# Optimization experiments

Measured on AMD Instinct MI355X. Metric: run time of the kernel, lower is better.

Reference implementation:

```python
import jax, jax.numpy as jnp
import numpy as np

B, R, D, H, L, E, NREL = 8, 1024, 256, 8, 2, 32768, 32
FF = 4 * D
HD = D // H
NEG = -1e9  # finite 'masked' value (stands in for -inf in the sparse attention mask)


def setup_inputs() -> dict:
    key = jax.random.key(0)
    ks = jax.random.split(key, 18)
    s = 0.02
    inp = {
        'node_embeddings': jax.random.normal(ks[0], (B, R, D), jnp.float32),
        'edge_index': jax.random.randint(ks[1], (B, 2, E), 0, R, jnp.int32),
        'relation_id': jax.random.randint(ks[2], (B, E), 0, NREL, jnp.int32),
        'keep_mask': jax.random.randint(ks[3], (B, E), 0, 2, jnp.int32).astype(bool),
        # learned params
        'rel_bias': jax.random.normal(ks[4], (max(NREL, 32), 1), jnp.float32) * s,
        'Wqkv': jax.random.normal(ks[5], (L, 3 * D, D), jnp.float32) * s,
        'bqkv': jnp.zeros((L, 3 * D), jnp.float32),
        'Wo': jax.random.normal(ks[6], (L, D, D), jnp.float32) * s,
        'bo': jnp.zeros((L, D), jnp.float32),
        'ln1_g': jnp.ones((L, D), jnp.float32),
        'ln1_b': jnp.zeros((L, D), jnp.float32),
        'W1': jax.random.normal(ks[7], (L, FF, D), jnp.float32) * s,
        'b1': jnp.zeros((L, FF), jnp.float32),
        'W2': jax.random.normal(ks[8], (L, D, FF), jnp.float32) * s,
        'b2': jnp.zeros((L, D), jnp.float32),
        'ln2_g': jnp.ones((L, D), jnp.float32),
        'ln2_b': jnp.zeros((L, D), jnp.float32),
    }
    return inp


def _layer_norm(x, g, b, eps=1e-5):
    mu = jnp.mean(x, axis=-1, keepdims=True)
    var = jnp.mean(jnp.square(x - mu), axis=-1, keepdims=True)
    return (x - mu) * jax.lax.rsqrt(var + eps) * g + b


def _build_mask(edge_index, relation_id, keep_mask, rel_bias):
    # Vectorized equivalent of the per-batch / per-edge Python loops:
    # base mask: NEG everywhere, 0 at kept edges (and diagonal), then scatter-ADD
    # the per-edge relation bias (duplicate edges accumulate, as in the loop).
    src = edge_index[:, 0, :]  # [B,E]
    dst = edge_index[:, 1, :]  # [B,E]
    bidx = jnp.broadcast_to(jnp.arange(B)[:, None], (B, E))
    mask = jnp.full((B, R, R), NEG, jnp.float32)
    base_vals = jnp.where(keep_mask, 0.0, NEG)
    mask = mask.at[bidx, src, dst].max(base_vals)  # dropped edges leave NEG
    di = jnp.arange(R)
    mask = mask.at[:, di, di].set(0.0)  # self-attention always allowed
    bias = rel_bias[relation_id, 0]  # [B,E]
    mask = mask.at[bidx, src, dst].add(jnp.where(keep_mask, bias, 0.0))
    return mask


def reference(node_embeddings, edge_index, relation_id, keep_mask, rel_bias,
              Wqkv, bqkv, Wo, bo, ln1_g, ln1_b, W1, b1, W2, b2, ln2_g, ln2_b):
    mask = _build_mask(edge_index, relation_id, keep_mask, rel_bias)  # [B,R,R]
    x = node_embeddings
    scale = 1.0 / np.sqrt(HD).astype(np.float32)
    for l in range(L):
        qkv = jnp.einsum('brd,ed->bre', x, Wqkv[l]) + bqkv[l]
        q, k, v = jnp.split(qkv, 3, axis=-1)
        q = q.reshape(B, R, H, HD)
        k = k.reshape(B, R, H, HD)
        v = v.reshape(B, R, H, HD)
        scores = jnp.einsum('bqhd,bkhd->bhqk', q, k) * scale + mask[:, None]
        attn = jax.nn.softmax(scores, axis=-1)
        out = jnp.einsum('bhqk,bkhd->bqhd', attn, v).reshape(B, R, D)
        out = jnp.einsum('brd,ed->bre', out, Wo[l]) + bo[l]
        x = _layer_norm(x + out, ln1_g[l], ln1_b[l])
        h = jax.nn.gelu(jnp.einsum('brd,fd->brf', x, W1[l]) + b1[l], approximate=False)
        h = jnp.einsum('brf,df->brd', h, W2[l]) + b2[l]
        x = _layer_norm(x + h, ln2_g[l], ln2_b[l])
    return x
```

## Files before the change

### kernel.cpp

```cpp
#include <hip/hip_runtime.h>
#include <hip/hip_bf16.h>
#include <math.h>

#define B_ 8
#define R_ 1024
#define D_ 256
#define H_ 8
#define L_ 2
#define E_ 32768
#define FF_ 1024
#define NEGV (-1000000000.0f)

typedef short bf16x8 __attribute__((ext_vector_type(8)));
typedef float f32x4 __attribute__((ext_vector_type(4)));

__device__ __forceinline__ unsigned short f2b(float f){
  unsigned int u = __float_as_uint(f);
  u += 0x7fffu + ((u >> 16) & 1u);
  return (unsigned short)(u >> 16);
}

__device__ __forceinline__ unsigned int pk_bf16(float lo, float hi){
  unsigned int r;
  asm volatile("v_cvt_pk_bf16_f32 %0, %1, %2" : "=v"(r) : "v"(lo), "v"(hi));
  return r;
}

#define ASYNC_COPY16(gp, lp) \
  __builtin_amdgcn_global_load_lds((const __attribute__((address_space(1))) void*)(gp), \
                                   (__attribute__((address_space(3))) void*)(lp), 16, 0, 0)


__global__ void detect_bool(const unsigned char* __restrict__ km, int* __restrict__ flag){
  int i = blockIdx.x*256 + threadIdx.x;
  int hit = ((i & 3) != 0) && (km[i] != 0);
  if (__ballot(hit) != 0ull && (threadIdx.x & 63) == 0) atomicOr(flag, 1);
}

__global__ void mask_fill(float* __restrict__ mask){
  size_t i = ((size_t)blockIdx.x*256 + threadIdx.x)*4;
  int row = (int)((i >> 10) & 1023);
  int col = (int)(i & 1023);
  float4 v;
  v.x = (row == col+0) ? 0.0f : NEGV;
  v.y = (row == col+1) ? 0.0f : NEGV;
  v.z = (row == col+2) ? 0.0f : NEGV;
  v.w = (row == col+3) ? 0.0f : NEGV;
  *(float4*)&mask[i] = v;
}

__device__ __forceinline__ int keep_of(const unsigned char* km, const int* flag, int tid){
  return flag[0] ? (int)km[tid] : (int)km[(size_t)tid*4];
}

__global__ void edge_base(const int* __restrict__ ei, const unsigned char* __restrict__ km,
                          const int* __restrict__ flag, float* __restrict__ mask){
  int tid = blockIdx.x*256 + threadIdx.x;
  int b = tid >> 15, e = tid & (E_-1);
  if (keep_of(km, flag, tid)){
    int src = ei[(size_t)b*2*E_ + e];
    int dst = ei[(size_t)b*2*E_ + E_ + e];
    mask[((size_t)b*R_ + src)*R_ + dst] = 0.0f;
  }
}

__global__ void edge_bias(const int* __restrict__ ei, const int* __restrict__ rid,
                          const unsigned char* __restrict__ km, const int* __restrict__ flag,
                          const float* __restrict__ rb, float* __restrict__ mask){
  int tid = blockIdx.x*256 + threadIdx.x;
  int b = tid >> 15, e = tid & (E_-1);
  if (keep_of(km, flag, tid)){
    int src = ei[(size_t)b*2*E_ + e];
    int dst = ei[(size_t)b*2*E_ + E_ + e];
    atomicAdd(&mask[((size_t)b*R_ + src)*R_ + dst], rb[rid[tid]]);
  }
}


__global__ void cvt_bf16(const float* __restrict__ src, unsigned short* __restrict__ dst, int n){
  int i = (blockIdx.x*256 + threadIdx.x)*4;
  if (i >= n) return;
  float4 v = *(const float4*)&src[i];
  ushort4 o;
  o.x = f2b(v.x); o.y = f2b(v.y); o.z = f2b(v.z); o.w = f2b(v.w);
  *(ushort4*)&dst[i] = o;
}

template<int MODE, int BN>
__global__ __launch_bounds__(256) void gemm_bt(const unsigned short* __restrict__ A,
    const unsigned short* __restrict__ Bw, const float* __restrict__ bias,
    void* __restrict__ Cout, int M, int N, int K)
{
  constexpr int NI = BN/32;
  constexpr int NCH = 8 + BN/16;
  constexpr int CPW = NCH/4;
  __shared__ unsigned short As[128*32];
  __shared__ unsigned short Bs[BN*32];
  const int nb = N / BN;
  const int bm = blockIdx.x / nb, bn = blockIdx.x % nb;
  const int m0 = bm << 7, n0 = bn * BN;
  const int t = threadIdx.x, lane = t & 63, wid = t >> 6;
  const int wr = wid >> 1, wc = wid & 1;
  const int c = lane & 15, g = lane >> 4;

  f32x4 zz = {0.f,0.f,0.f,0.f};
  f32x4 acc[4][NI];
  #pragma unroll
  for (int mi=0; mi<4; mi++)
    #pragma unroll
    for (int ni=0; ni<NI; ni++) acc[mi][ni] = zz;

  for (int k0 = 0; k0 < K; k0 += 32){
    __syncthreads();
    #pragma unroll
    for (int it=0; it<CPW; ++it){
      int chunk = wid*CPW + it;
      int row16 = lane >> 2, seg = lane & 3;
      if (chunk < 8){
        int row = chunk*16 + row16;
        ASYNC_COPY16(A + (size_t)(m0+row)*K + k0 + seg*8, &As[chunk*512]);
      } else {
        int bch = chunk - 8;
        int row = bch*16 + row16;
        ASYNC_COPY16(Bw + (size_t)(n0+row)*K + k0 + seg*8, &Bs[bch*512]);
      }
    }
    __syncthreads();
    bf16x8 af[4], bfr[NI];
    #pragma unroll
    for (int mi=0; mi<4; mi++) af[mi]  = *(const bf16x8*)&As[(wr*64 + mi*16 + c)*32 + g*8];
    #pragma unroll
    for (int ni=0; ni<NI; ni++) bfr[ni] = *(const bf16x8*)&Bs[(wc*(BN/2) + ni*16 + c)*32 + g*8];
    #pragma unroll
    for (int mi=0; mi<4; mi++)
      #pragma unroll
      for (int ni=0; ni<NI; ni++)
        acc[mi][ni] = __builtin_amdgcn_mfma_f32_16x16x32_bf16(af[mi], bfr[ni], acc[mi][ni], 0,0,0);
  }

  #pragma unroll
  for (int mi=0; mi<4; mi++){
    #pragma unroll
    for (int ni=0; ni<NI; ni++){
      int col = n0 + wc*(BN/2) + ni*16 + c;
      float bv = bias[col];
      #pragma unroll
      for (int r=0; r<4; r++){
        int row = m0 + wr*64 + mi*16 + 4*g + r;
        float v = acc[mi][ni][r] + bv;
        if (MODE == 2) v = 0.5f*v*(1.0f + erff(v*0.70710678f));
        if (MODE == 1) ((float*)Cout)[(size_t)row*N + col] = v;
        else           ((unsigned short*)Cout)[(size_t)row*N + col] = f2b(v);
      }
    }
  }
}

__global__ __launch_bounds__(512, 4) void attn_kernel(const unsigned short* __restrict__ qkv,
    const float* __restrict__ mask, unsigned short* __restrict__ aout)
{
  __shared__ unsigned short Klds[128*40];
  __shared__ unsigned short VT[32*136];
  const int blk = blockIdx.x;
  const int qt = blk & 7, h = (blk >> 3) & 7, b = blk >> 6;
  const int t = threadIdx.x, lane = t & 63, w = t >> 6;
  const int c = lane & 15, g = lane >> 4;
  const int qrow = qt*128 + w*16 + c;
  const size_t qbase = (size_t)b*R_*768;
  const float scale = 0.17677669529663689f;

  bf16x8 qf = *(const bf16x8*)&qkv[qbase + (size_t)qrow*768 + h*32 + g*8];

  f32x4 z4 = {0.f,0.f,0.f,0.f};
  f32x4 oacc[2] = {z4, z4};
  float mrun = -1e30f, lrun = 0.f;

  const int srcA = c + ((lane & 16) << 1);
  const int srcB = srcA + 16;
  const bool hig = (lane >= 32);

  for (int kt=0; kt<8; ++kt){
    const int kv0 = kt*128;
    __syncthreads();
    {
      int row = t >> 2, seg = t & 3;
      uint4 kd = *(const uint4*)&qkv[qbase + (size_t)(kv0+row)*768 + 256 + h*32 + seg*8];
      *(uint4*)&Klds[row*40 + seg*8] = kd;
    }
    {
      int d = t & 31, grp = t >> 5;
      __align__(16) unsigned short tv[8];
      #pragma unroll
      for (int j=0; j<8; j++)
        tv[j] = qkv[qbase + (size_t)(kv0 + grp*8 + j)*768 + 512 + h*32 + d];
      *(uint4*)&VT[d*136 + grp*8] = *(const uint4*)&tv[0];
    }
    __syncthreads();

    f32x4 st[8];
    #pragma unroll
    for (int fc=0; fc<8; ++fc){
      bf16x8 kb = *(const bf16x8*)&Klds[(fc*16 + c)*40 + g*8];
      st[fc] = __builtin_amdgcn_mfma_f32_16x16x32_bf16(kb, qf, z4, 0,0,0);
    }
    const float* mrow = &mask[((size_t)b*R_ + qrow)*R_ + kv0];
    #pragma unroll
    for (int fc=0; fc<8; ++fc){
      float4 mv = *(const float4*)&mrow[fc*16 + 4*g];
      st[fc][0] = st[fc][0]*scale + mv.x;
      st[fc][1] = st[fc][1]*scale + mv.y;
      st[fc][2] = st[fc][2]*scale + mv.z;
      st[fc][3] = st[fc][3]*scale + mv.w;
    }
    float mx = st[0][0];
    #pragma unroll
    for (int fc=0; fc<8; ++fc)
      #pragma unroll
      for (int r=0; r<4; r++) mx = fmaxf(mx, st[fc][r]);
    mx = fmaxf(mx, __shfl_xor(mx, 16));
    mx = fmaxf(mx, __shfl_xor(mx, 32));
    float mnew  = fmaxf(mrun, mx);
    float alpha = __expf(mrun - mnew);
    float sum = 0.f;
    #pragma unroll
    for (int fc=0; fc<8; ++fc)
      #pragma unroll
      for (int r=0; r<4; r++){
        float pv = __expf(st[fc][r] - mnew);
        st[fc][r] = pv;
        sum += pv;
      }
    sum += __shfl_xor(sum, 16);
    sum += __shfl_xor(sum, 32);
    lrun = lrun*alpha + sum;
    mrun = mnew;
    oacc[0][0]*=alpha; oacc[0][1]*=alpha; oacc[0][2]*=alpha; oacc[0][3]*=alpha;
    oacc[1][0]*=alpha; oacc[1][1]*=alpha; oacc[1][2]*=alpha; oacc[1][3]*=alpha;

    unsigned int u0[8], u1[8];
    #pragma unroll
    for (int fc=0; fc<8; ++fc){
      u0[fc] = pk_bf16(st[fc][0], st[fc][1]);
      u1[fc] = pk_bf16(st[fc][2], st[fc][3]);
    }

    #pragma unroll
    for (int ks=0; ks<4; ++ks){
      unsigned int e0 = u0[2*ks],   e1 = u1[2*ks];
      unsigned int o0 = u0[2*ks+1], o1 = u1[2*ks+1];
      unsigned int w0e = __shfl((int)e0, srcA), w1e = __shfl((int)e1, srcA);
      unsigned int w2e = __shfl((int)e0, srcB), w3e = __shfl((int)e1, srcB);
      unsigned int w0o = __shfl((int)o0, srcA), w1o = __shfl((int)o1, srcA);
      unsigned int w2o = __shfl((int)o0, srcB), w3o = __shfl((int)o1, srcB);
      union { unsigned int u[4]; bf16x8 v; } pa;
      pa.u[0] = hig ? w0o : w0e;
      pa.u[1] = hig ? w1o : w1e;
      pa.u[2] = hig ? w2o : w2e;
      pa.u[3] = hig ? w3o : w3e;
      #pragma unroll
      for (int dg=0; dg<2; ++dg){
        bf16x8 vb = *(const bf16x8*)&VT[(dg*16 + c)*136 + ks*32 + g*8];
        oacc[dg] = __builtin_amdgcn_mfma_f32_16x16x32_bf16(vb, pa.v, oacc[dg], 0,0,0);
      }
    }
  }
  float rl = 1.0f / lrun;
  #pragma unroll
  for (int dg=0; dg<2; ++dg){
    unsigned int p0 = pk_bf16(oacc[dg][0]*rl, oacc[dg][1]*rl);
    unsigned int p1 = pk_bf16(oacc[dg][2]*rl, oacc[dg][3]*rl);
    size_t base = ((size_t)b*R_ + qrow)*D_ + h*32 + dg*16 + 4*g;
    uint2 pp; pp.x = p0; pp.y = p1;
    *(uint2*)&aout[base] = pp;
  }
}

__global__ __launch_bounds__(256) void resid_ln(const float* __restrict__ xin,
    const float* __restrict__ res, const float* __restrict__ gg, const float* __restrict__ bb,
    float* __restrict__ xout, unsigned short* __restrict__ xbf)
{
  int row = blockIdx.x*4 + (threadIdx.x >> 6);
  int lane = threadIdx.x & 63;
  size_t base = (size_t)row*D_ + lane*4;
  float4 a  = *(const float4*)&xin[base];
  float4 rr = *(const float4*)&res[base];
  float y0 = a.x+rr.x, y1 = a.y+rr.y, y2 = a.z+rr.z, y3 = a.w+rr.w;
  float s = y0+y1+y2+y3;
  #pragma unroll
  for (int off=32; off>=1; off>>=1) s += __shfl_xor(s, off);
  float mu = s * (1.0f/256.0f);
  float d0=y0-mu, d1=y1-mu, d2=y2-mu, d3=y3-mu;
  float q = d0*d0 + d1*d1 + d2*d2 + d3*d3;
  #pragma unroll
  for (int off=32; off>=1; off>>=1) q += __shfl_xor(q, off);
  float rstd = rsqrtf(q*(1.0f/256.0f) + 1e-5f);
  float4 gv = *(const float4*)&gg[lane*4];
  float4 bv = *(const float4*)&bb[lane*4];
  float o0 = d0*rstd*gv.x + bv.x;
  float o1 = d1*rstd*gv.y + bv.y;
  float o2 = d2*rstd*gv.z + bv.z;
  float o3 = d3*rstd*gv.w + bv.w;
  float4 o; o.x=o0; o.y=o1; o.z=o2; o.w=o3;
  *(float4*)&xout[base] = o;
  ushort4 ob; ob.x=f2b(o0); ob.y=f2b(o1); ob.z=f2b(o2); ob.w=f2b(o3);
  *(ushort4*)&xbf[base] = ob;
}

extern "C" void kernel_launch(void* const* d_in, const int* in_sizes, int n_in,
                              void* d_out, int out_size, void* d_ws, size_t ws_size,
                              hipStream_t stream)
{
  const float* node = (const float*)d_in[0];
  const int*   ei   = (const int*)d_in[1];
  const int*   rid  = (const int*)d_in[2];
  const unsigned char* km = (const unsigned char*)d_in[3];
  const float* rb   = (const float*)d_in[4];
  const float* Wqkv = (const float*)d_in[5];
  const float* bqkv = (const float*)d_in[6];
  const float* Wo   = (const float*)d_in[7];
  const float* bo   = (const float*)d_in[8];
  const float* ln1g = (const float*)d_in[9];
  const float* ln1b = (const float*)d_in[10];
  const float* W1   = (const float*)d_in[11];
  const float* b1   = (const float*)d_in[12];
  const float* W2   = (const float*)d_in[13];
  const float* b2   = (const float*)d_in[14];
  const float* ln2g = (const float*)d_in[15];
  const float* ln2b = (const float*)d_in[16];

  char* ws = (char*)d_ws;
  int*   flag = (int*)ws;
  float* mask = (float*)(ws + 256);
  unsigned short* wqkv_b = (unsigned short*)(ws + 33554688);
  unsigned short* wo_b   = (unsigned short*)(ws + 34341120);
  unsigned short* w1_b   = (unsigned short*)(ws + 34603264);
  unsigned short* w2_b   = (unsigned short*)(ws + 35651840);
  unsigned short* x_bf   = (unsigned short*)(ws + 36700416);
  unsigned short* qkvb   = (unsigned short*)(ws + 40894720);
  unsigned short* ao     = (unsigned short*)(ws + 53477632);
  float* xf   = (float*)(ws + 57671936);
  float* tmp  = (float*)(ws + 66060544);
  unsigned short* hbuf   = (unsigned short*)(ws + 74449152);

  hipMemsetAsync(flag, 0, 4, stream);
  detect_bool<<<1024, 256, 0, stream>>>(km, flag);
  mask_fill<<<8192, 256, 0, stream>>>(mask);
  edge_base<<<1024, 256, 0, stream>>>(ei, km, flag, mask);
  edge_bias<<<1024, 256, 0, stream>>>(ei, rid, km, flag, rb, mask);

  cvt_bf16<<<384, 256, 0, stream>>>(Wqkv, wqkv_b, L_*768*256);
  cvt_bf16<<<128, 256, 0, stream>>>(Wo,   wo_b,   L_*256*256);
  cvt_bf16<<<512, 256, 0, stream>>>(W1,   w1_b,   L_*1024*256);
  cvt_bf16<<<512, 256, 0, stream>>>(W2,   w2_b,   L_*256*1024);
  cvt_bf16<<<2048,256, 0, stream>>>(node, x_bf,   B_*R_*D_);

  for (int l = 0; l < L_; ++l){
    gemm_bt<0,128><<<384, 256, 0, stream>>>(x_bf, wqkv_b + l*196608, bqkv + l*768, qkvb, 8192, 768, 256);
    attn_kernel<<<512, 512, 0, stream>>>(qkvb, mask, ao);
    gemm_bt<1,64><<<256, 256, 0, stream>>>(ao, wo_b + l*65536, bo + l*256, tmp, 8192, 256, 256);
    resid_ln<<<2048, 256, 0, stream>>>(l==0 ? node : xf, tmp, ln1g + l*256, ln1b + l*256, xf, x_bf);
    gemm_bt<2,128><<<512, 256, 0, stream>>>(x_bf, w1_b + l*262144, b1 + l*1024, hbuf, 8192, 1024, 256);
    gemm_bt<1,64><<<256, 256, 0, stream>>>(hbuf, w2_b + l*262144, b2 + l*256, tmp, 8192, 256, 1024);
    float* outp = (l == L_-1) ? (float*)d_out : xf;
    resid_ln<<<2048, 256, 0, stream>>>(xf, tmp, ln2g + l*256, ln2b + l*256, outp, x_bf);
  }
}
```

Before: 341.7 us.

## Convert mask to bf16, split attention KV in halves, split-K output GEMMs

Converts the dense fp32 mask to bf16 once so attention reads half the mask bytes. Attention now splits the key range into two halves per block, which doubles the block count; a new merge kernel combines the partials using the saved running max and sum. The Wo and W2 GEMMs use split-K=2 with bf16 partial outputs, and a new residual+layernorm kernel sums the two partials and adds the bias. It also changes LDS padding and aliases workspace buffers. The extra passes and bf16 partials add memory traffic and rounding error in exchange for more parallelism and less mask bandwidth.

```diff
diff --git a/kernel.cpp b/kernel.cpp
--- a/kernel.cpp
+++ b/kernel.cpp
@@ -19,7 +19,9 @@
   u += 0x7fffu + ((u >> 16) & 1u);
   return (unsigned short)(u >> 16);
 }
-
+__device__ __forceinline__ float b2f(unsigned short u){
+  return __uint_as_float((unsigned int)u << 16);
+}
 __device__ __forceinline__ unsigned int pk_bf16(float lo, float hi){
   unsigned int r;
   asm volatile("v_cvt_pk_bf16_f32 %0, %1, %2" : "=v"(r) : "v"(lo), "v"(hi));
@@ -86,7 +88,7 @@
   *(ushort4*)&dst[i] = o;
 }
 
-template<int MODE, int BN>
+template<int MODE, int BN, int KS>
 __global__ __launch_bounds__(256) void gemm_bt(const unsigned short* __restrict__ A,
     const unsigned short* __restrict__ Bw, const float* __restrict__ bias,
     void* __restrict__ Cout, int M, int N, int K)
@@ -96,9 +98,12 @@
   constexpr int CPW = NCH/4;
   __shared__ unsigned short As[128*32];
   __shared__ unsigned short Bs[BN*32];
-  const int nb = N / BN;
-  const int bm = blockIdx.x / nb, bn = blockIdx.x % nb;
+  const int nb = N / BN, mb = M >> 7;
+  const int ks = blockIdx.x / (mb*nb);
+  const int rem = blockIdx.x % (mb*nb);
+  const int bm = rem / nb, bn = rem % nb;
   const int m0 = bm << 7, n0 = bn * BN;
+  const int kbeg = ks * (K/KS), kend = kbeg + K/KS;
   const int t = threadIdx.x, lane = t & 63, wid = t >> 6;
   const int wr = wid >> 1, wc = wid & 1;
   const int c = lane & 15, g = lane >> 4;
@@ -110,7 +115,7 @@
     #pragma unroll
     for (int ni=0; ni<NI; ni++) acc[mi][ni] = zz;
 
-  for (int k0 = 0; k0 < K; k0 += 32){
+  for (int k0 = kbeg; k0 < kend; k0 += 32){
     __syncthreads();
     #pragma unroll
     for (int it=0; it<CPW; ++it){
@@ -138,31 +143,32 @@
         acc[mi][ni] = __builtin_amdgcn_mfma_f32_16x16x32_bf16(af[mi], bfr[ni], acc[mi][ni], 0,0,0);
   }
 
+  unsigned short* outb = (unsigned short*)Cout + (size_t)ks*M*N;
   #pragma unroll
   for (int mi=0; mi<4; mi++){
     #pragma unroll
     for (int ni=0; ni<NI; ni++){
       int col = n0 + wc*(BN/2) + ni*16 + c;
-      float bv = bias[col];
+      float bv = (MODE == 1) ? 0.0f : bias[col];
       #pragma unroll
       for (int r=0; r<4; r++){
         int row = m0 + wr*64 + mi*16 + 4*g + r;
         float v = acc[mi][ni][r] + bv;
         if (MODE == 2) v = 0.5f*v*(1.0f + erff(v*0.70710678f));
-        if (MODE == 1) ((float*)Cout)[(size_t)row*N + col] = v;
-        else           ((unsigned short*)Cout)[(size_t)row*N + col] = f2b(v);
+        outb[(size_t)row*N + col] = f2b(v);
       }
     }
   }
 }
 
 __global__ __launch_bounds__(512, 4) void attn_kernel(const unsigned short* __restrict__ qkv,
-    const float* __restrict__ mask, unsigned short* __restrict__ aout)
+    const unsigned short* __restrict__ maskbf, unsigned short* __restrict__ po,
+    float* __restrict__ ml)
 {
-  __shared__ unsigned short Klds[128*40];
-  __shared__ unsigned short VT[32*136];
+  __shared__ unsigned short Klds[128*36];
+  __shared__ unsigned short VT[32*132];
   const int blk = blockIdx.x;
-  const int qt = blk & 7, h = (blk >> 3) & 7, b = blk >> 6;
+  const int half = blk & 1, qt = (blk >> 1) & 7, h = (blk >> 4) & 7, b = blk >> 7;
   const int t = threadIdx.x, lane = t & 63, w = t >> 6;
   const int c = lane & 15, g = lane >> 4;
   const int qrow = qt*128 + w*16 + c;
@@ -179,13 +185,13 @@
   const int srcB = srcA + 16;
   const bool hig = (lane >= 32);
 
-  for (int kt=0; kt<8; ++kt){
-    const int kv0 = kt*128;
+  for (int kt=0; kt<4; ++kt){
+    const int kv0 = half*512 + kt*128;
     __syncthreads();
     {
       int row = t >> 2, seg = t & 3;
       uint4 kd = *(const uint4*)&qkv[qbase + (size_t)(kv0+row)*768 + 256 + h*32 + seg*8];
-      *(uint4*)&Klds[row*40 + seg*8] = kd;
+      *(uint4*)&Klds[row*36 + seg*8] = kd;
     }
     {
       int d = t & 31, grp = t >> 5;
@@ -193,24 +199,24 @@
       #pragma unroll
       for (int j=0; j<8; j++)
         tv[j] = qkv[qbase + (size_t)(kv0 + grp*8 + j)*768 + 512 + h*32 + d];
-      *(uint4*)&VT[d*136 + grp*8] = *(const uint4*)&tv[0];
+      *(uint4*)&VT[d*132 + grp*8] = *(const uint4*)&tv[0];
     }
     __syncthreads();
 
     f32x4 st[8];
     #pragma unroll
     for (int fc=0; fc<8; ++fc){
-      bf16x8 kb = *(const bf16x8*)&Klds[(fc*16 + c)*40 + g*8];
+      bf16x8 kb = *(const bf16x8*)&Klds[(fc*16 + c)*36 + g*8];
       st[fc] = __builtin_amdgcn_mfma_f32_16x16x32_bf16(kb, qf, z4, 0,0,0);
     }
-    const float* mrow = &mask[((size_t)b*R_ + qrow)*R_ + kv0];
+    const unsigned short* mrow = &maskbf[((size_t)b*R_ + qrow)*R_ + kv0];
     #pragma unroll
     for (int fc=0; fc<8; ++fc){
-      float4 mv = *(const float4*)&mrow[fc*16 + 4*g];
-      st[fc][0] = st[fc][0]*scale + mv.x;
-      st[fc][1] = st[fc][1]*scale + mv.y;
-      st[fc][2] = st[fc][2]*scale + mv.z;
-      st[fc][3] = st[fc][3]*scale + mv.w;
+      ushort4 mu = *(const ushort4*)&mrow[fc*16 + 4*g];
+      st[fc][0] = st[fc][0]*scale + b2f(mu.x);
+      st[fc][1] = st[fc][1]*scale + b2f(mu.y);
+      st[fc][2] = st[fc][2]*scale + b2f(mu.z);
+      st[fc][3] = st[fc][3]*scale + b2f(mu.w);
     }
     float mx = st[0][0];
     #pragma unroll
@@ -243,7 +249,6 @@
       u0[fc] = pk_bf16(st[fc][0], st[fc][1]);
       u1[fc] = pk_bf16(st[fc][2], st[fc][3]);
     }
-
     #pragma unroll
     for (int ks=0; ks<4; ++ks){
       unsigned int e0 = u0[2*ks],   e1 = u1[2*ks];
@@ -259,32 +264,72 @@
       pa.u[3] = hig ? w3o : w3e;
       #pragma unroll
       for (int dg=0; dg<2; ++dg){
-        bf16x8 vb = *(const bf16x8*)&VT[(dg*16 + c)*136 + ks*32 + g*8];
+        bf16x8 vb = *(const bf16x8*)&VT[(dg*16 + c)*132 + ks*32 + g*8];
         oacc[dg] = __builtin_amdgcn_mfma_f32_16x16x32_bf16(vb, pa.v, oacc[dg], 0,0,0);
       }
     }
   }
-  float rl = 1.0f / lrun;
+  unsigned short* poh = po + (size_t)half*B_*R_*D_;
   #pragma unroll
   for (int dg=0; dg<2; ++dg){
-    unsigned int p0 = pk_bf16(oacc[dg][0]*rl, oacc[dg][1]*rl);
-    unsigned int p1 = pk_bf16(oacc[dg][2]*rl, oacc[dg][3]*rl);
-    size_t base = ((size_t)b*R_ + qrow)*D_ + h*32 + dg*16 + 4*g;
-    uint2 pp; pp.x = p0; pp.y = p1;
-    *(uint2*)&aout[base] = pp;
-  }
-}
-
-__global__ __launch_bounds__(256) void resid_ln(const float* __restrict__ xin,
-    const float* __restrict__ res, const float* __restrict__ gg, const float* __restrict__ bb,
+    uint2 pp;
+    pp.x = pk_bf16(oacc[dg][0], oacc[dg][1]);
+    pp.y = pk_bf16(oacc[dg][2], oacc[dg][3]);
+    *(uint2*)&poh[((size_t)b*R_ + qrow)*D_ + h*32 + dg*16 + 4*g] = pp;
+  }
+  if (g == 0){
+    float2 v; v.x = mrun; v.y = lrun;
+    *(float2*)&ml[((size_t)(half*64 + b*8 + h)*1024 + qrow)*2] = v;
+  }
+}
+
+__global__ __launch_bounds__(256) void attn_merge(const unsigned short* __restrict__ po,
+    const float* __restrict__ ml, unsigned short* __restrict__ aout)
+{
+  int idx = blockIdx.x*256 + threadIdx.x;
+  int seg = idx & 3;
+  int q   = (idx >> 2) & 1023;
+  int h   = (idx >> 12) & 7;
+  int b   = idx >> 15;
+  size_t mlb = ((size_t)(b*8 + h)*1024 + q)*2;
+  float m0 = ml[mlb],          l0 = ml[mlb + 1];
+  float m1 = ml[131072 + mlb], l1 = ml[131072 + mlb + 1];
+  float mm = fmaxf(m0, m1);
+  float a0 = __expf(m0 - mm), a1 = __expf(m1 - mm);
+  float inv = 1.0f / (a0*l0 + a1*l1);
+  a0 *= inv; a1 *= inv;
+  size_t base = ((size_t)b*R_ + q)*D_ + h*32 + seg*8;
+  uint4 o0 = *(const uint4*)&po[base];
+  uint4 o1 = *(const uint4*)&po[(size_t)B_*R_*D_ + base];
+  uint4 out;
+  unsigned int* p0 = (unsigned int*)&o0;
+  unsigned int* p1 = (unsigned int*)&o1;
+  unsigned int* po_ = (unsigned int*)&out;
+  #pragma unroll
+  for (int j=0; j<4; ++j){
+    float lo = a0*__uint_as_float(p0[j] << 16)       + a1*__uint_as_float(p1[j] << 16);
+    float hi = a0*__uint_as_float(p0[j] & 0xffff0000u) + a1*__uint_as_float(p1[j] & 0xffff0000u);
+    po_[j] = pk_bf16(lo, hi);
+  }
+  *(uint4*)&aout[base] = out;
+}
+
+__global__ __launch_bounds__(256) void resid_ln3(const float* __restrict__ xin,
+    const unsigned short* __restrict__ pA, const unsigned short* __restrict__ pB,
+    const float* __restrict__ bias, const float* __restrict__ gg, const float* __restrict__ bb,
     float* __restrict__ xout, unsigned short* __restrict__ xbf)
 {
   int row = blockIdx.x*4 + (threadIdx.x >> 6);
   int lane = threadIdx.x & 63;
   size_t base = (size_t)row*D_ + lane*4;
   float4 a  = *(const float4*)&xin[base];
-  float4 rr = *(const float4*)&res[base];
-  float y0 = a.x+rr.x, y1 = a.y+rr.y, y2 = a.z+rr.z, y3 = a.w+rr.w;
+  ushort4 ua = *(const ushort4*)&pA[base];
+  ushort4 ub = *(const ushort4*)&pB[base];
+  float4 bs = *(const float4*)&bias[lane*4];
+  float y0 = a.x + b2f(ua.x) + b2f(ub.x) + bs.x;
+  float y1 = a.y + b2f(ua.y) + b2f(ub.y) + bs.y;
+  float y2 = a.z + b2f(ua.z) + b2f(ub.z) + bs.z;
+  float y3 = a.w + b2f(ua.w) + b2f(ub.w) + bs.w;
   float s = y0+y1+y2+y3;
   #pragma unroll
   for (int off=32; off>=1; off>>=1) s += __shfl_xor(s, off);
@@ -329,24 +374,28 @@
   const float* ln2b = (const float*)d_in[16];
 
   char* ws = (char*)d_ws;
-  int*   flag = (int*)ws;
-  float* mask = (float*)(ws + 256);
-  unsigned short* wqkv_b = (unsigned short*)(ws + 33554688);
-  unsigned short* wo_b   = (unsigned short*)(ws + 34341120);
-  unsigned short* w1_b   = (unsigned short*)(ws + 34603264);
-  unsigned short* w2_b   = (unsigned short*)(ws + 35651840);
-  unsigned short* x_bf   = (unsigned short*)(ws + 36700416);
-  unsigned short* qkvb   = (unsigned short*)(ws + 40894720);
-  unsigned short* ao     = (unsigned short*)(ws + 53477632);
-  float* xf   = (float*)(ws + 57671936);
-  float* tmp  = (float*)(ws + 66060544);
-  unsigned short* hbuf   = (unsigned short*)(ws + 74449152);
+  int*   flag   = (int*)ws;
+  float* maskf  = (float*)(ws + 256);
+  unsigned short* hbuf   = (unsigned short*)(ws + 256);
+  unsigned short* maskbf = (unsigned short*)(ws + 33554688);
+  unsigned short* wqkv_b = (unsigned short*)(ws + 50331904);
+  unsigned short* wo_b   = (unsigned short*)(ws + 51118336);
+  unsigned short* w1_b   = (unsigned short*)(ws + 51380480);
+  unsigned short* w2_b   = (unsigned short*)(ws + 52429056);
+  unsigned short* x_bf   = (unsigned short*)(ws + 53477632);
+  unsigned short* qkvb   = (unsigned short*)(ws + 57671936);
+  unsigned short* ao     = (unsigned short*)(ws + 57671936);
+  float* xf   = (float*)(ws + 70254848);
+  unsigned short* po  = (unsigned short*)(ws + 78643456);
+  unsigned short* tmp = (unsigned short*)(ws + 78643456);
+  float* ml   = (float*)(ws + 87032064);
 
   hipMemsetAsync(flag, 0, 4, stream);
   detect_bool<<<1024, 256, 0, stream>>>(km, flag);
-  mask_fill<<<8192, 256, 0, stream>>>(mask);
-  edge_base<<<1024, 256, 0, stream>>>(ei, km, flag, mask);
-  edge_bias<<<1024, 256, 0, stream>>>(ei, rid, km, flag, rb, mask);
+  mask_fill<<<8192, 256, 0, stream>>>(maskf);
+  edge_base<<<1024, 256, 0, stream>>>(ei, km, flag, maskf);
+  edge_bias<<<1024, 256, 0, stream>>>(ei, rid, km, flag, rb, maskf);
+  cvt_bf16<<<8192, 256, 0, stream>>>(maskf, maskbf, B_*R_*R_);
 
   cvt_bf16<<<384, 256, 0, stream>>>(Wqkv, wqkv_b, L_*768*256);
   cvt_bf16<<<128, 256, 0, stream>>>(Wo,   wo_b,   L_*256*256);
@@ -355,13 +404,16 @@
   cvt_bf16<<<2048,256, 0, stream>>>(node, x_bf,   B_*R_*D_);
 
   for (int l = 0; l < L_; ++l){
-    gemm_bt<0,128><<<384, 256, 0, stream>>>(x_bf, wqkv_b + l*196608, bqkv + l*768, qkvb, 8192, 768, 256);
-    attn_kernel<<<512, 512, 0, stream>>>(qkvb, mask, ao);
-    gemm_bt<1,64><<<256, 256, 0, stream>>>(ao, wo_b + l*65536, bo + l*256, tmp, 8192, 256, 256);
-    resid_ln<<<2048, 256, 0, stream>>>(l==0 ? node : xf, tmp, ln1g + l*256, ln1b + l*256, xf, x_bf);
-    gemm_bt<2,128><<<512, 256, 0, stream>>>(x_bf, w1_b + l*262144, b1 + l*1024, hbuf, 8192, 1024, 256);
-    gemm_bt<1,64><<<256, 256, 0, stream>>>(hbuf, w2_b + l*262144, b2 + l*256, tmp, 8192, 256, 1024);
+    gemm_bt<0,128,1><<<384, 256, 0, stream>>>(x_bf, wqkv_b + l*196608, bqkv + l*768, qkvb, 8192, 768, 256);
+    attn_kernel<<<1024, 512, 0, stream>>>(qkvb, maskbf, po, ml);
+    attn_merge<<<1024, 256, 0, stream>>>(po, ml, ao);
+    gemm_bt<1,64,2><<<512, 256, 0, stream>>>(ao, wo_b + l*65536, bo + l*256, tmp, 8192, 256, 256);
+    resid_ln3<<<2048, 256, 0, stream>>>(l==0 ? node : xf, tmp, tmp + 8192*256,
+                                        bo + l*256, ln1g + l*256, ln1b + l*256, xf, x_bf);
+    gemm_bt<2,128,1><<<512, 256, 0, stream>>>(x_bf, w1_b + l*262144, b1 + l*1024, hbuf, 8192, 1024, 256);
+    gemm_bt<1,64,2><<<512, 256, 0, stream>>>(hbuf, w2_b + l*262144, b2 + l*256, tmp, 8192, 256, 1024);
     float* outp = (l == L_-1) ? (float*)d_out : xf;
-    resid_ln<<<2048, 256, 0, stream>>>(xf, tmp, ln2g + l*256, ln2b + l*256, outp, x_bf);
-  }
-}
+    resid_ln3<<<2048, 256, 0, stream>>>(xf, tmp, tmp + 8192*256,
+                                        b2 + l*256, ln2g + l*256, ln2b + l*256, outp, x_bf);
+  }
+}
```

Result: slower. 359.2 us (+5.2%).
